# Optimization experiments

Hardware: AMD Instinct MI355X
Metric: run time of the kernel (lower is better)

## Reference

```python
import jax, jax.numpy as jnp
import numpy as np

PRO_NUM, MAX_LEN, HID = 64, 1024, 256
TERM_NUM = 512


def setup_inputs() -> dict:
    key = jax.random.key(0)
    k1, k2, k3 = jax.random.split(key, 3)
    term_encoding = jax.random.normal(k1, (TERM_NUM, HID), dtype=jnp.float32)
    pro_encoding = jax.random.normal(k2, (PRO_NUM, MAX_LEN, HID), dtype=jnp.float32)
    # lengths in [1, MAX_LEN] so no row is fully masked (avoids NaN softmax)
    pro_lens = jax.random.randint(k3, (PRO_NUM,), 1, MAX_LEN + 1)
    return {"term_encoding": term_encoding, "pro_encoding": pro_encoding, "pro_lens": pro_lens}


def reference(term_encoding, pro_encoding, pro_lens):
    # scores: pro_num x term_num x max_len  (QK^T without sqrt(d) scaling, as in original)
    scores = jnp.einsum("plh,th->ptl", pro_encoding, term_encoding)
    max_len = pro_encoding.shape[1]
    # mask positions >= pro_lens (per protein), broadcast over term dim
    mask = jnp.arange(max_len)[None, None, :] >= pro_lens[:, None, None]  # p,1,l
    scores = jnp.where(mask, -jnp.inf, scores)
    attn = jax.nn.softmax(scores, axis=-1)  # pro_num x term_num x max_len
    out = jnp.einsum("ptl,plh->pth", attn, pro_encoding)  # pro_num x term_num x hid
    return (out, attn)
```

## Files before the change

### kernel.cpp

```cpp
#include <hip/hip_runtime.h>

#define PRO_NUM 64
#define TERM_NUM 512
#define MAX_LEN 1024
#define HID 256

typedef _Float16 f16x8 __attribute__((ext_vector_type(8)));
typedef _Float16 f16x4 __attribute__((ext_vector_type(4)));
typedef float f32x4 __attribute__((ext_vector_type(4)));


__device__ __forceinline__ f16x8 cvt8(const float* __restrict__ s) {
  float4 a = *(const float4*)s;
  float4 b = *(const float4*)(s + 4);
  f16x8 r = {(_Float16)a.x, (_Float16)a.y, (_Float16)a.z, (_Float16)a.w,
             (_Float16)b.x, (_Float16)b.y, (_Float16)b.z, (_Float16)b.w};
  return r;
}

__global__ __launch_bounds__(256) void k_prep(const float* __restrict__ pro,
                                              f16x8* __restrict__ fragP,
                                              f16x8* __restrict__ fragT) {
  __shared__ _Float16 ldsA[64][264];
  const int p = blockIdx.y;
  const int lc = blockIdx.x;
  const int tid = threadIdx.x;

  const float* src = pro + ((size_t)p * MAX_LEN + lc * 64) * HID;
  #pragma unroll
  for (int j = 0; j < 16; ++j) {
    int idx = j * 1024 + tid * 4;
    int l = idx >> 8, h = idx & 255;
    float4 v = *(const float4*)(src + idx);
    ldsA[l][h + 0] = (_Float16)v.x;
    ldsA[l][h + 1] = (_Float16)v.y;
    ldsA[l][h + 2] = (_Float16)v.z;
    ldsA[l][h + 3] = (_Float16)v.w;
  }
  __syncthreads();

  const int w = tid >> 6;
  const int lane = tid & 63;
  const int lr = lane & 15;
  const int lg = lane >> 4;

  {
    const int T = lc * 4 + w;
    f16x8* dst = fragP + ((size_t)(p * 64 + T) * 8) * 64 + lane;
    #pragma unroll
    for (int kk = 0; kk < 8; ++kk)
      dst[kk * 64] = *(const f16x8*)&ldsA[w * 16 + lr][kk * 32 + lg * 8];
  }
  #pragma unroll
  for (int hh = 0; hh < 4; ++hh) {
    const int H = w * 4 + hh;
    #pragma unroll
    for (int k2 = 0; k2 < 2; ++k2) {
      const int kc = lc * 2 + k2;
      const int lloc = k2 * 32 + lg * 8;
      f16x8 v;
      #pragma unroll
      for (int i = 0; i < 8; ++i) v[i] = ldsA[lloc + i][H * 16 + lr];
      fragT[((size_t)(p * 16 + H) * 32 + kc) * 64 + lane] = v;
    }
  }
}

__global__ __launch_bounds__(256) void k_fused(
    const float* __restrict__ term, const f16x8* __restrict__ fragP,
    const f16x8* __restrict__ fragT, const int* __restrict__ lens,
    float* __restrict__ attn, float* __restrict__ out) {
  __shared__ __align__(16) _Float16 attn_lds[32][1024];
  __shared__ float rmx[4][32];
  __shared__ float rsm[4][32];

  const int bid = blockIdx.x;
  const int swz = (bid & 7) * 128 + (bid >> 3);
  const int p = swz >> 4;
  const int t0 = (swz & 15) * 32;

  const int tid = threadIdx.x;
  const int w = tid >> 6;
  const int lane = tid & 63;
  const int lr = lane & 15;
  const int lg = lane >> 4;
  const int len = lens[p];
  const int l0w = w * 256;

  f32x4 acc[2][16];
  #pragma unroll
  for (int mt = 0; mt < 2; ++mt)
    #pragma unroll
    for (int i = 0; i < 16; ++i) acc[mt][i] = (f32x4){0.f, 0.f, 0.f, 0.f};

  const float* trow0 = term + (size_t)(t0 + lr) * HID + lg * 8;
  const f16x8* pbw = fragP + ((size_t)(p * 64 + w * 16) * 8) * 64 + lane;

  #pragma unroll
  for (int kk = 0; kk < 8; ++kk) {
    f16x8 a0 = cvt8(trow0 + kk * 32);
    f16x8 a1 = cvt8(trow0 + (size_t)16 * HID + kk * 32);
    f16x8 bf[16];
    #pragma unroll
    for (int tile = 0; tile < 16; ++tile) bf[tile] = pbw[(tile * 8 + kk) * 64];
    #pragma unroll
    for (int tile = 0; tile < 16; ++tile) {
      acc[0][tile] = __builtin_amdgcn_mfma_f32_16x16x32_f16(a0, bf[tile], acc[0][tile], 0, 0, 0);
      acc[1][tile] = __builtin_amdgcn_mfma_f32_16x16x32_f16(a1, bf[tile], acc[1][tile], 0, 0, 0);
    }
  }

  float rmax[2][4];
  #pragma unroll
  for (int mt = 0; mt < 2; ++mt)
    #pragma unroll
    for (int r = 0; r < 4; ++r) rmax[mt][r] = -INFINITY;

  #pragma unroll
  for (int tile = 0; tile < 16; ++tile) {
    int l = l0w + tile * 16 + lr;
    #pragma unroll
    for (int mt = 0; mt < 2; ++mt) {
      #pragma unroll
      for (int r = 0; r < 4; ++r) {
        float s = (l < len) ? acc[mt][tile][r] : -INFINITY;
        acc[mt][tile][r] = s;
        rmax[mt][r] = fmaxf(rmax[mt][r], s);
      }
    }
  }
  #pragma unroll
  for (int m = 1; m < 16; m <<= 1) {
    #pragma unroll
    for (int mt = 0; mt < 2; ++mt)
      #pragma unroll
      for (int r = 0; r < 4; ++r) rmax[mt][r] = fmaxf(rmax[mt][r], __shfl_xor(rmax[mt][r], m));
  }
  if (lr == 0) {
    #pragma unroll
    for (int mt = 0; mt < 2; ++mt)
      #pragma unroll
      for (int r = 0; r < 4; ++r) rmx[w][mt * 16 + lg * 4 + r] = rmax[mt][r];
  }
  __syncthreads();
  float fm[2][4];
  #pragma unroll
  for (int mt = 0; mt < 2; ++mt)
    #pragma unroll
    for (int r = 0; r < 4; ++r) {
      int row = mt * 16 + lg * 4 + r;
      fm[mt][r] = fmaxf(fmaxf(rmx[0][row], rmx[1][row]), fmaxf(rmx[2][row], rmx[3][row]));
    }

  float rsum[2][4] = {{0.f, 0.f, 0.f, 0.f}, {0.f, 0.f, 0.f, 0.f}};
  #pragma unroll
  for (int tile = 0; tile < 16; ++tile) {
    #pragma unroll
    for (int mt = 0; mt < 2; ++mt) {
      #pragma unroll
      for (int r = 0; r < 4; ++r) {
        float e = __expf(acc[mt][tile][r] - fm[mt][r]);
        acc[mt][tile][r] = e;
        rsum[mt][r] += e;
      }
    }
  }
  #pragma unroll
  for (int m = 1; m < 16; m <<= 1) {
    #pragma unroll
    for (int mt = 0; mt < 2; ++mt)
      #pragma unroll
      for (int r = 0; r < 4; ++r) rsum[mt][r] += __shfl_xor(rsum[mt][r], m);
  }
  if (lr == 0) {
    #pragma unroll
    for (int mt = 0; mt < 2; ++mt)
      #pragma unroll
      for (int r = 0; r < 4; ++r) rsm[w][mt * 16 + lg * 4 + r] = rsum[mt][r];
  }
  __syncthreads();
  float inv[2][4];
  #pragma unroll
  for (int mt = 0; mt < 2; ++mt)
    #pragma unroll
    for (int r = 0; r < 4; ++r) {
      int row = mt * 16 + lg * 4 + r;
      inv[mt][r] = 1.0f / (rsm[0][row] + rsm[1][row] + rsm[2][row] + rsm[3][row]);
    }

  #pragma unroll
  for (int mt = 0; mt < 2; ++mt) {
    #pragma unroll
    for (int r = 0; r < 4; ++r) {
      const int row = mt * 16 + lg * 4 + r;
      float* arow = attn + ((size_t)(p * TERM_NUM + t0 + row)) * MAX_LEN + l0w + lr;
      const int sw = (row & 7) << 3;
      #pragma unroll
      for (int tile = 0; tile < 16; ++tile) {
        float v = acc[mt][tile][r] * inv[mt][r];
        __builtin_nontemporal_store(v, &arow[tile * 16]);
        attn_lds[row][(l0w + tile * 16 + lr) ^ sw] = (_Float16)v;
      }
    }
  }
  __syncthreads();

  f32x4 acc2[2][4];
  #pragma unroll
  for (int mt = 0; mt < 2; ++mt)
    #pragma unroll
    for (int nt = 0; nt < 4; ++nt) acc2[mt][nt] = (f32x4){0.f, 0.f, 0.f, 0.f};

  const f16x8* btw = fragT + ((size_t)(p * 16 + w * 4) * 32) * 64 + lane;
  const int kcmax = (len + 31) >> 5;

  #pragma unroll 4
  for (int kc = 0; kc < kcmax; ++kc) {
    const int k0 = kc * 32;
    f16x8 a[2];
    #pragma unroll
    for (int mt = 0; mt < 2; ++mt) {
      const int row = mt * 16 + lr;
      a[mt] = *(const f16x8*)&attn_lds[row][(k0 + lg * 8) ^ ((row & 7) << 3)];
    }
    #pragma unroll
    for (int nt = 0; nt < 4; ++nt) {
      f16x8 bf = btw[(nt * 32 + kc) * 64];
      acc2[0][nt] = __builtin_amdgcn_mfma_f32_16x16x32_f16(a[0], bf, acc2[0][nt], 0, 0, 0);
      acc2[1][nt] = __builtin_amdgcn_mfma_f32_16x16x32_f16(a[1], bf, acc2[1][nt], 0, 0, 0);
    }
  }

  #pragma unroll
  for (int mt = 0; mt < 2; ++mt) {
    #pragma unroll
    for (int nt = 0; nt < 4; ++nt) {
      #pragma unroll
      for (int r = 0; r < 4; ++r) {
        __builtin_nontemporal_store(
            acc2[mt][nt][r],
            &out[((size_t)p * TERM_NUM + t0 + mt * 16 + lg * 4 + r) * HID + w * 64 + nt * 16 + lr]);
      }
    }
  }
}

extern "C" void kernel_launch(void* const* d_in, const int* in_sizes, int n_in,
                              void* d_out, int out_size, void* d_ws, size_t ws_size,
                              hipStream_t stream) {
  const float* term = (const float*)d_in[0];
  const float* pro  = (const float*)d_in[1];
  const int*   lens = (const int*)d_in[2];

  float* out  = (float*)d_out;
  float* attn = out + (size_t)PRO_NUM * TERM_NUM * HID;

  f16x8* fragP = (f16x8*)d_ws;
  f16x8* fragT = fragP + (size_t)PRO_NUM * 64 * 8 * 64;

  k_prep<<<dim3(MAX_LEN / 64, PRO_NUM), 256, 0, stream>>>(pro, fragP, fragT);
  k_fused<<<dim3(PRO_NUM * (TERM_NUM / 32)), 256, 0, stream>>>(term, fragP, fragT, lens, attn, out);
}
```

Before: 131.0 us.

## Coalesce attn stores via LDS and skip QK tiles beyond sequence length

Writes the attention matrix row-wise from the LDS fp16 buffer using vectorized 16-byte nontemporal stores instead of per-element strided stores from MFMA registers. It also skips the QK MFMA work for groups of 8 tiles that lie fully past the protein length, and preloads the B fragments in the PV loop. The attn output is now rounded through fp16 before being written as fp32, which reduces its precision.

Result: slower. 159.9 us (+22.1%).

```diff
diff --git a/kernel.cpp b/kernel.cpp
--- a/kernel.cpp
+++ b/kernel.cpp
@@ -87,6 +87,10 @@
   const int len = lens[p];
   const int l0w = w * 256;
 
+  int rem = len - l0w;
+  int ntiles = rem <= 0 ? 0 : ((rem + 15) >> 4);
+  if (ntiles > 16) ntiles = 16;
+
   f32x4 acc[2][16];
   #pragma unroll
   for (int mt = 0; mt < 2; ++mt)
@@ -97,16 +101,23 @@
   const f16x8* pbw = fragP + ((size_t)(p * 64 + w * 16) * 8) * 64 + lane;
 
   #pragma unroll
-  for (int kk = 0; kk < 8; ++kk) {
-    f16x8 a0 = cvt8(trow0 + kk * 32);
-    f16x8 a1 = cvt8(trow0 + (size_t)16 * HID + kk * 32);
-    f16x8 bf[16];
-    #pragma unroll
-    for (int tile = 0; tile < 16; ++tile) bf[tile] = pbw[(tile * 8 + kk) * 64];
-    #pragma unroll
-    for (int tile = 0; tile < 16; ++tile) {
-      acc[0][tile] = __builtin_amdgcn_mfma_f32_16x16x32_f16(a0, bf[tile], acc[0][tile], 0, 0, 0);
-      acc[1][tile] = __builtin_amdgcn_mfma_f32_16x16x32_f16(a1, bf[tile], acc[1][tile], 0, 0, 0);
+  for (int g = 0; g < 2; ++g) {
+    if (ntiles > g * 8) {
+      #pragma unroll
+      for (int kk = 0; kk < 8; ++kk) {
+        f16x8 a0 = cvt8(trow0 + kk * 32);
+        f16x8 a1 = cvt8(trow0 + (size_t)16 * HID + kk * 32);
+        f16x8 bf[8];
+        #pragma unroll
+        for (int t = 0; t < 8; ++t) bf[t] = pbw[((g * 8 + t) * 8 + kk) * 64];
+        #pragma unroll
+        for (int t = 0; t < 8; ++t) {
+          acc[0][g * 8 + t] =
+              __builtin_amdgcn_mfma_f32_16x16x32_f16(a0, bf[t], acc[0][g * 8 + t], 0, 0, 0);
+          acc[1][g * 8 + t] =
+              __builtin_amdgcn_mfma_f32_16x16x32_f16(a1, bf[t], acc[1][g * 8 + t], 0, 0, 0);
+        }
+      }
     }
   }
 
@@ -193,17 +204,30 @@
     #pragma unroll
     for (int r = 0; r < 4; ++r) {
       const int row = mt * 16 + lg * 4 + r;
-      float* arow = attn + ((size_t)(p * TERM_NUM + t0 + row)) * MAX_LEN + l0w + lr;
       const int sw = (row & 7) << 3;
       #pragma unroll
       for (int tile = 0; tile < 16; ++tile) {
-        float v = acc[mt][tile][r] * inv[mt][r];
-        __builtin_nontemporal_store(v, &arow[tile * 16]);
-        attn_lds[row][(l0w + tile * 16 + lr) ^ sw] = (_Float16)v;
-      }
-    }
-  }
-  __syncthreads();
+        attn_lds[row][(l0w + tile * 16 + lr) ^ sw] = (_Float16)(acc[mt][tile][r] * inv[mt][r]);
+      }
+    }
+  }
+  __syncthreads();
+
+  #pragma unroll
+  for (int i = 0; i < 8; ++i) {
+    const int row = w * 8 + i;
+    const int sw = (row & 7) << 3;
+    float* arow = attn + ((size_t)(p * TERM_NUM + t0 + row)) * MAX_LEN;
+    #pragma unroll
+    for (int pass = 0; pass < 2; ++pass) {
+      const int c0 = pass * 512 + lane * 8;
+      f16x8 v = *(const f16x8*)&attn_lds[row][c0 ^ sw];
+      f32x4 o0 = {(float)v[0], (float)v[1], (float)v[2], (float)v[3]};
+      f32x4 o1 = {(float)v[4], (float)v[5], (float)v[6], (float)v[7]};
+      __builtin_nontemporal_store(o0, (f32x4*)(arow + c0));
+      __builtin_nontemporal_store(o1, (f32x4*)(arow + c0 + 4));
+    }
+  }
 
   f32x4 acc2[2][4];
   #pragma unroll
@@ -217,6 +241,9 @@
   #pragma unroll 4
   for (int kc = 0; kc < kcmax; ++kc) {
     const int k0 = kc * 32;
+    f16x8 bf[4];
+    #pragma unroll
+    for (int nt = 0; nt < 4; ++nt) bf[nt] = btw[(nt * 32 + kc) * 64];
     f16x8 a[2];
     #pragma unroll
     for (int mt = 0; mt < 2; ++mt) {
@@ -225,9 +252,8 @@
     }
     #pragma unroll
     for (int nt = 0; nt < 4; ++nt) {
-      f16x8 bf = btw[(nt * 32 + kc) * 64];
-      acc2[0][nt] = __builtin_amdgcn_mfma_f32_16x16x32_f16(a[0], bf, acc2[0][nt], 0, 0, 0);
-      acc2[1][nt] = __builtin_amdgcn_mfma_f32_16x16x32_f16(a[1], bf, acc2[1][nt], 0, 0, 0);
+      acc2[0][nt] = __builtin_amdgcn_mfma_f32_16x16x32_f16(a[0], bf[nt], acc2[0][nt], 0, 0, 0);
+      acc2[1][nt] = __builtin_amdgcn_mfma_f32_16x16x32_f16(a[1], bf[nt], acc2[1][nt], 0, 0, 0);
     }
   }
 
```

## Split fused attention kernel into separate QK-softmax and PV kernels

Applied to the files above, without the earlier changes.

Splits the fused kernel in two. The first computes scores, applies the softmax and writes attn to global memory. The second reads attn back from global memory, converts it to fp16, and runs the PV matmul with an 8-chunk unrolled loop. This removes the 64KB LDS buffer and the barrier, which may raise occupancy in both kernels. In exchange the large attn tensor is read back from global memory after being written with nontemporal stores, and there is an extra launch.

Measured after the change: 192.8 us. 47.2% more time.

```diff
diff --git a/kernel.cpp b/kernel.cpp
--- a/kernel.cpp
+++ b/kernel.cpp
@@ -66,11 +66,9 @@
   }
 }
 
-__global__ __launch_bounds__(256) void k_fused(
+__global__ __launch_bounds__(256) void k_qk(
     const float* __restrict__ term, const f16x8* __restrict__ fragP,
-    const f16x8* __restrict__ fragT, const int* __restrict__ lens,
-    float* __restrict__ attn, float* __restrict__ out) {
-  __shared__ __align__(16) _Float16 attn_lds[32][1024];
+    const int* __restrict__ lens, float* __restrict__ attn) {
   __shared__ float rmx[4][32];
   __shared__ float rsm[4][32];
 
@@ -179,31 +177,37 @@
       for (int r = 0; r < 4; ++r) rsm[w][mt * 16 + lg * 4 + r] = rsum[mt][r];
   }
   __syncthreads();
-  float inv[2][4];
-  #pragma unroll
-  for (int mt = 0; mt < 2; ++mt)
-    #pragma unroll
-    for (int r = 0; r < 4; ++r) {
-      int row = mt * 16 + lg * 4 + r;
-      inv[mt][r] = 1.0f / (rsm[0][row] + rsm[1][row] + rsm[2][row] + rsm[3][row]);
-    }
 
   #pragma unroll
   for (int mt = 0; mt < 2; ++mt) {
     #pragma unroll
     for (int r = 0; r < 4; ++r) {
       const int row = mt * 16 + lg * 4 + r;
+      const float inv =
+          1.0f / (rsm[0][row] + rsm[1][row] + rsm[2][row] + rsm[3][row]);
       float* arow = attn + ((size_t)(p * TERM_NUM + t0 + row)) * MAX_LEN + l0w + lr;
-      const int sw = (row & 7) << 3;
       #pragma unroll
       for (int tile = 0; tile < 16; ++tile) {
-        float v = acc[mt][tile][r] * inv[mt][r];
-        __builtin_nontemporal_store(v, &arow[tile * 16]);
-        attn_lds[row][(l0w + tile * 16 + lr) ^ sw] = (_Float16)v;
-      }
-    }
-  }
-  __syncthreads();
+        __builtin_nontemporal_store(acc[mt][tile][r] * inv, &arow[tile * 16]);
+      }
+    }
+  }
+}
+
+__global__ __launch_bounds__(256) void k_pv(
+    const float* __restrict__ attn, const f16x8* __restrict__ fragT,
+    const int* __restrict__ lens, float* __restrict__ out) {
+  const int bid = blockIdx.x;
+  const int swz = (bid & 7) * 128 + (bid >> 3);
+  const int p = swz >> 4;
+  const int t0 = (swz & 15) * 32;
+
+  const int tid = threadIdx.x;
+  const int w = tid >> 6;
+  const int lane = tid & 63;
+  const int lr = lane & 15;
+  const int lg = lane >> 4;
+  const int len = lens[p];
 
   f32x4 acc2[2][4];
   #pragma unroll
@@ -211,23 +215,27 @@
     #pragma unroll
     for (int nt = 0; nt < 4; ++nt) acc2[mt][nt] = (f32x4){0.f, 0.f, 0.f, 0.f};
 
+  const float* arow0 = attn + ((size_t)(p * TERM_NUM + t0 + lr)) * MAX_LEN + lg * 8;
+  const float* arow1 = arow0 + (size_t)16 * MAX_LEN;
   const f16x8* btw = fragT + ((size_t)(p * 16 + w * 4) * 32) * 64 + lane;
-  const int kcmax = (len + 31) >> 5;
-
-  #pragma unroll 4
-  for (int kc = 0; kc < kcmax; ++kc) {
-    const int k0 = kc * 32;
-    f16x8 a[2];
-    #pragma unroll
-    for (int mt = 0; mt < 2; ++mt) {
-      const int row = mt * 16 + lr;
-      a[mt] = *(const f16x8*)&attn_lds[row][(k0 + lg * 8) ^ ((row & 7) << 3)];
-    }
-    #pragma unroll
-    for (int nt = 0; nt < 4; ++nt) {
-      f16x8 bf = btw[(nt * 32 + kc) * 64];
-      acc2[0][nt] = __builtin_amdgcn_mfma_f32_16x16x32_f16(a[0], bf, acc2[0][nt], 0, 0, 0);
-      acc2[1][nt] = __builtin_amdgcn_mfma_f32_16x16x32_f16(a[1], bf, acc2[1][nt], 0, 0, 0);
+
+  const int ngroups = (((len + 31) >> 5) + 7) >> 3;
+
+  for (int g = 0; g < ngroups; ++g) {
+    #pragma unroll
+    for (int u = 0; u < 8; ++u) {
+      const int kc = g * 8 + u;
+      const int k0 = kc * 32;
+      f16x8 bf[4];
+      #pragma unroll
+      for (int nt = 0; nt < 4; ++nt) bf[nt] = btw[(nt * 32 + kc) * 64];
+      f16x8 a0 = cvt8(arow0 + k0);
+      f16x8 a1 = cvt8(arow1 + k0);
+      #pragma unroll
+      for (int nt = 0; nt < 4; ++nt) {
+        acc2[0][nt] = __builtin_amdgcn_mfma_f32_16x16x32_f16(a0, bf[nt], acc2[0][nt], 0, 0, 0);
+        acc2[1][nt] = __builtin_amdgcn_mfma_f32_16x16x32_f16(a1, bf[nt], acc2[1][nt], 0, 0, 0);
+      }
     }
   }
 
@@ -259,5 +267,6 @@
   f16x8* fragT = fragP + (size_t)PRO_NUM * 64 * 8 * 64;
 
   k_prep<<<dim3(MAX_LEN / 64, PRO_NUM), 256, 0, stream>>>(pro, fragP, fragT);
-  k_fused<<<dim3(PRO_NUM * (TERM_NUM / 32)), 256, 0, stream>>>(term, fragP, fragT, lens, attn, out);
-}
+  k_qk<<<dim3(PRO_NUM * (TERM_NUM / 32)), 256, 0, stream>>>(term, fragP, lens, attn);
+  k_pv<<<dim3(PRO_NUM * (TERM_NUM / 32)), 256, 0, stream>>>(attn, fragT, lens, out);
+}
```
